# Kernel tuning notes

Measured on AMD Instinct MI355X. Metric: run time of the kernel, lower is better.

## Reference

```python
import math
import jax, jax.numpy as jnp
import numpy as np

EPS = 1e-05        # self.eps
EPS_VAR = 1e-04    # self.eps_var
NORM_EPS = 1e-12   # F.normalize default eps


def _gelu_tanh(x):
    c = math.sqrt(2.0 / math.pi)
    return 0.5 * x * (1.0 + jnp.tanh(c * (x + 0.044715 * x ** 3)))


def _l2_normalize(v, axis=-1):
    # matches F.normalize: v / max(||v||, 1e-12)
    n = jnp.sqrt(jnp.sum(v * v, axis=axis, keepdims=True))
    return v / jnp.maximum(n, NORM_EPS)


def setup_inputs() -> dict:
    key = jax.random.key(0)
    B, T, D = 4, 4096, 2048
    x = jax.random.normal(key, (B, T, D), dtype=jnp.float32)
    return {
        "x": x,
        "log_tau": jnp.asarray(math.log(2.0), dtype=jnp.float32),
        "log_sigma_raw": jnp.asarray(math.log(math.exp(0.5) - 1.0), dtype=jnp.float32),
        "log_w_raw": jnp.asarray(math.log(math.exp(1.0) - 1.0), dtype=jnp.float32),
    }


def reference(x, log_tau, log_sigma_raw, log_w_raw):
    B, T, D = x.shape
    tau = jnp.exp(log_tau)
    sigma = jax.nn.softplus(log_sigma_raw)
    w = jax.nn.softplus(log_w_raw)

    out = _gelu_tanh(x)

    # ----- causal running stats (detached in original) -----
    xd = jax.lax.stop_gradient(x)
    outd = jax.lax.stop_gradient(out)

    zeros_1 = jnp.zeros((B, 1, D), dtype=x.dtype)
    # exclusive (causal) cumulative sums along T
    cum_x = jnp.concatenate([zeros_1, jnp.cumsum(xd, axis=1)[:, :-1, :]], axis=1)
    cum_xsq = jnp.concatenate([zeros_1, jnp.cumsum(xd * xd, axis=1)[:, :-1, :]], axis=1)
    cum_out = jnp.concatenate([zeros_1, jnp.cumsum(outd, axis=1)[:, :-1, :]], axis=1)

    counts = jnp.arange(1, T + 1, dtype=x.dtype).reshape(1, T, 1)  # >= 1 already
    mu = cum_x / counts
    sq_m = cum_xsq / counts
    var = jnp.maximum(sq_m - mu * mu, EPS_VAR)
    std = jnp.sqrt(var)

    z = (xd - mu) / (std + EPS)
    mean_abs_z = jnp.mean(jnp.abs(z), axis=-1)                  # [B, T]
    mask_1d = (counts[:, :, 0] > 1).astype(x.dtype)             # [1, T]
    mean_abs_z_masked = mean_abs_z * mask_1d

    mu_out = cum_out / counts
    out_n = _l2_normalize(outd, axis=-1)
    mu_out_n = _l2_normalize(mu_out, axis=-1)
    cos = jnp.sum(out_n * mu_out_n, axis=-1) * mask_1d          # [B, T]

    surp = jnp.tanh(sigma * mean_abs_z_masked)
    gate = jnp.exp(-tau * cos) * (1.0 + w * surp)               # [B, T]
    return out * gate[..., None]
```

## Files before the change

### kernel.cpp

```cpp
#include <hip/hip_runtime.h>
#include <math.h>

#define B_ 4
#define T_ 4096
#define D_ 2048
#define CT 32
#define NC (T_ / CT)

__device__ __forceinline__ float fast_tanh(float u) {
    float e = __expf(2.0f * u);
    return 1.0f - 2.0f / (e + 1.0f);
}

__device__ __forceinline__ float gelu_tanh(float x) {
    const float c = 0.7978845608028654f;
    float u = c * (x + 0.044715f * x * x * x);
    return 0.5f * x * (1.0f + fast_tanh(u));
}

__global__ __launch_bounds__(256) void k1_partials(
        const float* __restrict__ x,
        float* __restrict__ px, float* __restrict__ pxx, float* __restrict__ po) {
    int bid = blockIdx.x;
    int b = bid / NC, c = bid % NC;
    int tid = threadIdx.x;
    int d0 = tid * 8;
    float sx[8], sxx[8], so[8];
#pragma unroll
    for (int i = 0; i < 8; i++) { sx[i] = 0.f; sxx[i] = 0.f; so[i] = 0.f; }

    const float* base = x + ((size_t)(b * T_ + c * CT)) * D_ + d0;
    for (int t = 0; t < CT; t++) {
        float4 v0 = *(const float4*)(base);
        float4 v1 = *(const float4*)(base + 4);
        float v[8] = {v0.x, v0.y, v0.z, v0.w, v1.x, v1.y, v1.z, v1.w};
#pragma unroll
        for (int i = 0; i < 8; i++) {
            sx[i]  += v[i];
            sxx[i] += v[i] * v[i];
            so[i]  += gelu_tanh(v[i]);
        }
        base += D_;
    }
    size_t pidx = (size_t)(b * NC + c) * D_ + d0;
    *(float4*)(px  + pidx)     = make_float4(sx[0], sx[1], sx[2], sx[3]);
    *(float4*)(px  + pidx + 4) = make_float4(sx[4], sx[5], sx[6], sx[7]);
    *(float4*)(pxx + pidx)     = make_float4(sxx[0], sxx[1], sxx[2], sxx[3]);
    *(float4*)(pxx + pidx + 4) = make_float4(sxx[4], sxx[5], sxx[6], sxx[7]);
    *(float4*)(po  + pidx)     = make_float4(so[0], so[1], so[2], so[3]);
    *(float4*)(po  + pidx + 4) = make_float4(so[4], so[5], so[6], so[7]);
}

__global__ __launch_bounds__(256) void k2_scan(
        float* __restrict__ px, float* __restrict__ pxx, float* __restrict__ po) {
    int gid = blockIdx.x * blockDim.x + threadIdx.x;
    int b = gid / D_, d = gid % D_;
    float rx = 0.f, rxx = 0.f, ro = 0.f;
    size_t idx = (size_t)b * NC * D_ + d;
    for (int c = 0; c < NC; c++) {
        float tx = px[idx], txx = pxx[idx], to = po[idx];
        px[idx] = rx; pxx[idx] = rxx; po[idx] = ro;
        rx += tx; rxx += txx; ro += to;
        idx += D_;
    }
}

__global__ __launch_bounds__(256) void k3_main(
        const float* __restrict__ x,
        const float* __restrict__ px, const float* __restrict__ pxx,
        const float* __restrict__ po,
        const float* __restrict__ p_log_tau,
        const float* __restrict__ p_log_sigma_raw,
        const float* __restrict__ p_log_w_raw,
        float* __restrict__ y) {
    __shared__ float4 red[4];

    int bid = blockIdx.x;
    int b = bid / NC, c = bid % NC;
    int tid = threadIdx.x;
    int d0 = tid * 8;

    float tau   = __expf(p_log_tau[0]);
    float sigma = log1pf(__expf(p_log_sigma_raw[0]));
    float w     = log1pf(__expf(p_log_w_raw[0]));

    float cx[8], cxx[8], co[8];
    size_t pidx = (size_t)(b * NC + c) * D_ + d0;
    {
        float4 a0 = *(const float4*)(px  + pidx);
        float4 a1 = *(const float4*)(px  + pidx + 4);
        float4 b0 = *(const float4*)(pxx + pidx);
        float4 b1 = *(const float4*)(pxx + pidx + 4);
        float4 c0 = *(const float4*)(po  + pidx);
        float4 c1 = *(const float4*)(po  + pidx + 4);
        cx[0]=a0.x; cx[1]=a0.y; cx[2]=a0.z; cx[3]=a0.w;
        cx[4]=a1.x; cx[5]=a1.y; cx[6]=a1.z; cx[7]=a1.w;
        cxx[0]=b0.x; cxx[1]=b0.y; cxx[2]=b0.z; cxx[3]=b0.w;
        cxx[4]=b1.x; cxx[5]=b1.y; cxx[6]=b1.z; cxx[7]=b1.w;
        co[0]=c0.x; co[1]=c0.y; co[2]=c0.z; co[3]=c0.w;
        co[4]=c1.x; co[5]=c1.y; co[6]=c1.z; co[7]=c1.w;
    }

    const float* xb = x + ((size_t)(b * T_ + c * CT)) * D_ + d0;
    float*       yb = y + ((size_t)(b * T_ + c * CT)) * D_ + d0;

    for (int t = 0; t < CT; t++) {
        int tg = c * CT + t;
        float nf = (float)(tg + 1);
        float inv = __builtin_amdgcn_rcpf(nf);

        float4 v0 = *(const float4*)(xb);
        float4 v1 = *(const float4*)(xb + 4);
        float v[8] = {v0.x, v0.y, v0.z, v0.w, v1.x, v1.y, v1.z, v1.w};

        float o[8];
        float a_absz = 0.f, a_dot = 0.f, a_no2 = 0.f, a_nm2 = 0.f;
#pragma unroll
        for (int i = 0; i < 8; i++) {
            float vv = v[i];
            float oo = gelu_tanh(vv);
            o[i] = oo;
            float mu  = cx[i]  * inv;
            float sq  = cxx[i] * inv;
            float var = fmaxf(sq - mu * mu, 1e-4f);
            float stde = __builtin_amdgcn_sqrtf(var) + 1e-5f;
            float z = (vv - mu) * __builtin_amdgcn_rcpf(stde);
            a_absz += fabsf(z);
            float mo = co[i] * inv;
            a_dot += oo * mo;
            a_no2 += oo * oo;
            a_nm2 += mo * mo;
            cx[i]  += vv;
            cxx[i] += vv * vv;
            co[i]  += oo;
        }

#pragma unroll
        for (int off = 32; off >= 1; off >>= 1) {
            a_absz += __shfl_down(a_absz, off);
            a_dot  += __shfl_down(a_dot,  off);
            a_no2  += __shfl_down(a_no2,  off);
            a_nm2  += __shfl_down(a_nm2,  off);
        }
        int wid = tid >> 6;
        __syncthreads();
        if ((tid & 63) == 0) red[wid] = make_float4(a_absz, a_dot, a_no2, a_nm2);
        __syncthreads();
        float s_absz = 0.f, s_dot = 0.f, s_no2 = 0.f, s_nm2 = 0.f;
#pragma unroll
        for (int k = 0; k < 4; k++) {
            float4 r = red[k];
            s_absz += r.x; s_dot += r.y; s_no2 += r.z; s_nm2 += r.w;
        }

        float mask = (tg >= 1) ? 1.0f : 0.0f;
        float mabs = s_absz * (1.0f / (float)D_) * mask;
        float denom = fmaxf(sqrtf(s_no2), 1e-12f) * fmaxf(sqrtf(s_nm2), 1e-12f);
        float cosv = (s_dot / denom) * mask;
        float gate = __expf(-tau * cosv) * (1.0f + w * fast_tanh(sigma * mabs));

        *(float4*)(yb)     = make_float4(o[0]*gate, o[1]*gate, o[2]*gate, o[3]*gate);
        *(float4*)(yb + 4) = make_float4(o[4]*gate, o[5]*gate, o[6]*gate, o[7]*gate);

        xb += D_; yb += D_;
    }
}

extern "C" void kernel_launch(void* const* d_in, const int* in_sizes, int n_in,
                              void* d_out, int out_size, void* d_ws, size_t ws_size,
                              hipStream_t stream) {
    const float* x   = (const float*)d_in[0];
    const float* lt  = (const float*)d_in[1];
    const float* lsr = (const float*)d_in[2];
    const float* lwr = (const float*)d_in[3];
    float* y = (float*)d_out;

    const size_t npart = (size_t)B_ * NC * D_;
    float* px  = (float*)d_ws;
    float* pxx = px  + npart;
    float* po  = pxx + npart;

    k1_partials<<<B_ * NC, 256, 0, stream>>>(x, px, pxx, po);
    k2_scan<<<(B_ * D_) / 256, 256, 0, stream>>>(px, pxx, po);
    k3_main<<<B_ * NC, 256, 0, stream>>>(x, px, pxx, po, lt, lsr, lwr, y);
}
```

Measured before the change: 310.8 us.

## Parallelize chunk scan in two levels, batch block reductions over four rows, cheaper GELU

The serial per-column scan over 128 chunks becomes two passes: group sums over 8 groups, then a per-group scan that first adds the preceding group totals, giving 8x more threads. The main kernel now reduces four rows per barrier round instead of one, so the number of __syncthreads and shuffle chains drops fourfold, at the cost of more registers. GELU is rewritten algebraically as x - x/(e+1) with hardware reciprocals. The extra workspace and launch add some overhead, and the fast reciprocals change rounding slightly.

```diff
diff --git a/kernel.cpp b/kernel.cpp
--- a/kernel.cpp
+++ b/kernel.cpp
@@ -6,16 +6,21 @@
 #define D_ 2048
 #define CT 32
 #define NC (T_ / CT)
+#define NG 8
+#define GC (NC / NG)
+
+__device__ __forceinline__ float fast_rcp(float x) { return __builtin_amdgcn_rcpf(x); }
 
 __device__ __forceinline__ float fast_tanh(float u) {
     float e = __expf(2.0f * u);
-    return 1.0f - 2.0f / (e + 1.0f);
+    return 1.0f - 2.0f * fast_rcp(e + 1.0f);
 }
 
 __device__ __forceinline__ float gelu_tanh(float x) {
     const float c = 0.7978845608028654f;
-    float u = c * (x + 0.044715f * x * x * x);
-    return 0.5f * x * (1.0f + fast_tanh(u));
+    float u = c * x * fmaf(0.044715f, x * x, 1.0f);
+    float e = __expf(2.0f * u);
+    return x - x * fast_rcp(e + 1.0f);
 }
 
 __global__ __launch_bounds__(256) void k1_partials(
@@ -37,7 +42,7 @@
 #pragma unroll
         for (int i = 0; i < 8; i++) {
             sx[i]  += v[i];
-            sxx[i] += v[i] * v[i];
+            sxx[i]  = fmaf(v[i], v[i], sxx[i]);
             so[i]  += gelu_tanh(v[i]);
         }
         base += D_;
@@ -51,17 +56,47 @@
     *(float4*)(po  + pidx + 4) = make_float4(so[4], so[5], so[6], so[7]);
 }
 
-__global__ __launch_bounds__(256) void k2_scan(
-        float* __restrict__ px, float* __restrict__ pxx, float* __restrict__ po) {
-    int gid = blockIdx.x * blockDim.x + threadIdx.x;
-    int b = gid / D_, d = gid % D_;
-    float rx = 0.f, rxx = 0.f, ro = 0.f;
-    size_t idx = (size_t)b * NC * D_ + d;
-    for (int c = 0; c < NC; c++) {
-        float tx = px[idx], txx = pxx[idx], to = po[idx];
-        px[idx] = rx; pxx[idx] = rxx; po[idx] = ro;
-        rx += tx; rxx += txx; ro += to;
-        idx += D_;
+__global__ __launch_bounds__(256) void k2a_group_sums(
+        const float* __restrict__ px, const float* __restrict__ pxx,
+        const float* __restrict__ po,
+        float* __restrict__ gx, float* __restrict__ gxx, float* __restrict__ go) {
+    int gid = blockIdx.x * 256 + threadIdx.x;
+    int d = gid & (D_ - 1);
+    int g = (gid >> 11) & (NG - 1);
+    int b = gid >> 14;
+    size_t base = ((size_t)(b * NC + g * GC)) * D_ + d;
+    float sx = 0.f, sxx = 0.f, so = 0.f;
+#pragma unroll
+    for (int j = 0; j < GC; j++) {
+        sx  += px [base + (size_t)j * D_];
+        sxx += pxx[base + (size_t)j * D_];
+        so  += po [base + (size_t)j * D_];
+    }
+    size_t gi = ((size_t)(b * NG + g)) * D_ + d;
+    gx[gi] = sx; gxx[gi] = sxx; go[gi] = so;
+}
+
+__global__ __launch_bounds__(256) void k2c_scan(
+        float* __restrict__ px, float* __restrict__ pxx, float* __restrict__ po,
+        const float* __restrict__ gx, const float* __restrict__ gxx,
+        const float* __restrict__ go) {
+    int gid = blockIdx.x * 256 + threadIdx.x;
+    int d = gid & (D_ - 1);
+    int g = (gid >> 11) & (NG - 1);
+    int b = gid >> 14;
+
+    float ox = 0.f, oxx = 0.f, oo = 0.f;
+    for (int g2 = 0; g2 < g; g2++) {
+        size_t gi = ((size_t)(b * NG + g2)) * D_ + d;
+        ox += gx[gi]; oxx += gxx[gi]; oo += go[gi];
+    }
+    size_t base = ((size_t)(b * NC + g * GC)) * D_ + d;
+#pragma unroll
+    for (int j = 0; j < GC; j++) {
+        float tx = px[base], txx = pxx[base], to = po[base];
+        px[base] = ox; pxx[base] = oxx; po[base] = oo;
+        ox += tx; oxx += txx; oo += to;
+        base += D_;
     }
 }
 
@@ -73,7 +108,8 @@
         const float* __restrict__ p_log_sigma_raw,
         const float* __restrict__ p_log_w_raw,
         float* __restrict__ y) {
-    __shared__ float4 red[4];
+    __shared__ float red[4 * 16];
+    __shared__ float gates[4];
 
     int bid = blockIdx.x;
     int b = bid / NC, c = bid % NC;
@@ -104,65 +140,80 @@
     const float* xb = x + ((size_t)(b * T_ + c * CT)) * D_ + d0;
     float*       yb = y + ((size_t)(b * T_ + c * CT)) * D_ + d0;
 
-    for (int t = 0; t < CT; t++) {
-        int tg = c * CT + t;
-        float nf = (float)(tg + 1);
-        float inv = __builtin_amdgcn_rcpf(nf);
-
-        float4 v0 = *(const float4*)(xb);
-        float4 v1 = *(const float4*)(xb + 4);
-        float v[8] = {v0.x, v0.y, v0.z, v0.w, v1.x, v1.y, v1.z, v1.w};
-
-        float o[8];
-        float a_absz = 0.f, a_dot = 0.f, a_no2 = 0.f, a_nm2 = 0.f;
-#pragma unroll
-        for (int i = 0; i < 8; i++) {
-            float vv = v[i];
-            float oo = gelu_tanh(vv);
-            o[i] = oo;
-            float mu  = cx[i]  * inv;
-            float sq  = cxx[i] * inv;
-            float var = fmaxf(sq - mu * mu, 1e-4f);
-            float stde = __builtin_amdgcn_sqrtf(var) + 1e-5f;
-            float z = (vv - mu) * __builtin_amdgcn_rcpf(stde);
-            a_absz += fabsf(z);
-            float mo = co[i] * inv;
-            a_dot += oo * mo;
-            a_no2 += oo * oo;
-            a_nm2 += mo * mo;
-            cx[i]  += vv;
-            cxx[i] += vv * vv;
-            co[i]  += oo;
+    for (int r = 0; r < CT / 4; r++) {
+        float acc[16];
+#pragma unroll
+        for (int k = 0; k < 16; k++) acc[k] = 0.f;
+        float o[4][8];
+
+#pragma unroll
+        for (int t = 0; t < 4; t++) {
+            int tg = c * CT + r * 4 + t;
+            float inv = fast_rcp((float)(tg + 1));
+            const float* xr = xb + (size_t)(r * 4 + t) * D_;
+            float4 v0 = *(const float4*)(xr);
+            float4 v1 = *(const float4*)(xr + 4);
+            float v[8] = {v0.x, v0.y, v0.z, v0.w, v1.x, v1.y, v1.z, v1.w};
+#pragma unroll
+            for (int i = 0; i < 8; i++) {
+                float vv = v[i];
+                float oo = gelu_tanh(vv);
+                o[t][i] = oo;
+                float mu = cx[i] * inv;
+                float sq = cxx[i] * inv;
+                float var = fmaxf(fmaf(-mu, mu, sq), 1e-4f);
+                float stde = __builtin_amdgcn_sqrtf(var) + 1e-5f;
+                float z = (vv - mu) * fast_rcp(stde);
+                acc[t * 4 + 0] += fabsf(z);
+                float mo = co[i] * inv;
+                acc[t * 4 + 1] = fmaf(oo, mo, acc[t * 4 + 1]);
+                acc[t * 4 + 2] = fmaf(oo, oo, acc[t * 4 + 2]);
+                acc[t * 4 + 3] = fmaf(mo, mo, acc[t * 4 + 3]);
+                cx[i] += vv;
+                cxx[i] = fmaf(vv, vv, cxx[i]);
+                co[i] += oo;
+            }
         }
 
 #pragma unroll
         for (int off = 32; off >= 1; off >>= 1) {
-            a_absz += __shfl_down(a_absz, off);
-            a_dot  += __shfl_down(a_dot,  off);
-            a_no2  += __shfl_down(a_no2,  off);
-            a_nm2  += __shfl_down(a_nm2,  off);
-        }
-        int wid = tid >> 6;
+#pragma unroll
+            for (int k = 0; k < 16; k++) acc[k] += __shfl_down(acc[k], off);
+        }
+
         __syncthreads();
-        if ((tid & 63) == 0) red[wid] = make_float4(a_absz, a_dot, a_no2, a_nm2);
+        if ((tid & 63) == 0) {
+            int wbase = (tid >> 6) * 16;
+#pragma unroll
+            for (int k = 0; k < 16; k++) red[wbase + k] = acc[k];
+        }
         __syncthreads();
-        float s_absz = 0.f, s_dot = 0.f, s_no2 = 0.f, s_nm2 = 0.f;
-#pragma unroll
-        for (int k = 0; k < 4; k++) {
-            float4 r = red[k];
-            s_absz += r.x; s_dot += r.y; s_no2 += r.z; s_nm2 += r.w;
-        }
-
-        float mask = (tg >= 1) ? 1.0f : 0.0f;
-        float mabs = s_absz * (1.0f / (float)D_) * mask;
-        float denom = fmaxf(sqrtf(s_no2), 1e-12f) * fmaxf(sqrtf(s_nm2), 1e-12f);
-        float cosv = (s_dot / denom) * mask;
-        float gate = __expf(-tau * cosv) * (1.0f + w * fast_tanh(sigma * mabs));
-
-        *(float4*)(yb)     = make_float4(o[0]*gate, o[1]*gate, o[2]*gate, o[3]*gate);
-        *(float4*)(yb + 4) = make_float4(o[4]*gate, o[5]*gate, o[6]*gate, o[7]*gate);
-
-        xb += D_; yb += D_;
+        if (tid < 4) {
+            int t = tid;
+            float s0 = 0.f, s1 = 0.f, s2 = 0.f, s3 = 0.f;
+#pragma unroll
+            for (int wv = 0; wv < 4; wv++) {
+                s0 += red[wv * 16 + t * 4 + 0];
+                s1 += red[wv * 16 + t * 4 + 1];
+                s2 += red[wv * 16 + t * 4 + 2];
+                s3 += red[wv * 16 + t * 4 + 3];
+            }
+            int tg = c * CT + r * 4 + t;
+            float mask = (tg >= 1) ? 1.0f : 0.0f;
+            float mabs = s0 * (1.0f / (float)D_) * mask;
+            float denom = fmaxf(sqrtf(s2), 1e-12f) * fmaxf(sqrtf(s3), 1e-12f);
+            float cosv = (s1 * fast_rcp(denom)) * mask;
+            gates[t] = __expf(-tau * cosv) * (1.0f + w * fast_tanh(sigma * mabs));
+        }
+        __syncthreads();
+
+#pragma unroll
+        for (int t = 0; t < 4; t++) {
+            float g = gates[t];
+            float* yr = yb + (size_t)(r * 4 + t) * D_;
+            *(float4*)(yr)     = make_float4(o[t][0]*g, o[t][1]*g, o[t][2]*g, o[t][3]*g);
+            *(float4*)(yr + 4) = make_float4(o[t][4]*g, o[t][5]*g, o[t][6]*g, o[t][7]*g);
+        }
     }
 }
 
@@ -176,11 +227,16 @@
     float* y = (float*)d_out;
 
     const size_t npart = (size_t)B_ * NC * D_;
+    const size_t ngrp  = (size_t)B_ * NG * D_;
     float* px  = (float*)d_ws;
     float* pxx = px  + npart;
     float* po  = pxx + npart;
+    float* gx  = po  + npart;
+    float* gxx = gx  + ngrp;
+    float* go  = gxx + ngrp;
 
     k1_partials<<<B_ * NC, 256, 0, stream>>>(x, px, pxx, po);
-    k2_scan<<<(B_ * D_) / 256, 256, 0, stream>>>(px, pxx, po);
+    k2a_group_sums<<<(B_ * NG * D_) / 256, 256, 0, stream>>>(px, pxx, po, gx, gxx, go);
+    k2c_scan<<<(B_ * NG * D_) / 256, 256, 0, stream>>>(px, pxx, po, gx, gxx, go);
     k3_main<<<B_ * NC, 256, 0, stream>>>(x, px, pxx, po, lt, lsr, lwr, y);
 }
```

Result: faster. 285.4 us (-8.1%).
